# Performance work log

Measured on AMD Instinct MI355X. Metric: run time of the kernel, lower is better.

Reference implementation:

```python
import jax, jax.numpy as jnp
import numpy as np

N_NODES = 50000
N_EDGES = 800000
IN_DIM = 128
HIDDEN = 128
NUM_CLASSES = 64
NEG_SLOPE = 0.2


def setup_inputs() -> dict:
    key = jax.random.key(0)
    ks = jax.random.split(key, 12)
    x = jax.random.normal(ks[0], (N_NODES, IN_DIM), dtype=jnp.float32)
    src = jax.random.randint(ks[1], (N_EDGES,), 0, N_NODES, dtype=jnp.int64)
    dst = jax.random.randint(ks[2], (N_EDGES,), 0, N_NODES, dtype=jnp.int64)
    def glorot(k, shape):
        fan_in, fan_out = shape[0], shape[-1]
        s = jnp.sqrt(2.0 / (fan_in + fan_out)).astype(jnp.float32)
        return jax.random.normal(k, shape, dtype=jnp.float32) * s
    return {
        "x": x, "src": src, "dst": dst,
        # GATConv params (1 head, no bias, no residual)
        "W_gat": glorot(ks[3], (IN_DIM, HIDDEN)),
        "attn_l": glorot(ks[4], (HIDDEN,)),
        "attn_r": glorot(ks[5], (HIDDEN,)),
        # GraphConv params (norm='none', bias=True)
        "W1": glorot(ks[6], (HIDDEN, HIDDEN)),
        "b1": jnp.zeros((HIDDEN,), dtype=jnp.float32),
        "W2": glorot(ks[7], (HIDDEN, HIDDEN)),
        "b2": jnp.zeros((HIDDEN,), dtype=jnp.float32),
        "Wc": glorot(ks[8], (HIDDEN, NUM_CLASSES)),
        "bc": jnp.zeros((NUM_CLASSES,), dtype=jnp.float32),
    }


def reference(x, src, dst, W_gat, attn_l, attn_r, W1, b1, W2, b2, Wc, bc):
    N = x.shape[0]
    # --- GATConv, single head, eval mode (dropout=0) ---
    h = x @ W_gat                      # (N, H)
    el = h @ attn_l                    # (N,)
    er = h @ attn_r                    # (N,)
    e = jax.nn.leaky_relu(el[src] + er[dst], negative_slope=NEG_SLOPE)  # (E,)
    # edge softmax over incoming edges of each dst node
    emax = jax.ops.segment_max(e, dst, num_segments=N)
    ee = jnp.exp(e - emax[dst])
    esum = jax.ops.segment_sum(ee, dst, num_segments=N)
    alpha = ee / esum[dst]             # (E,) attention = reused edge weights
    h1 = jax.ops.segment_sum(h[src] * alpha[:, None], dst, num_segments=N)
    h1 = jax.nn.elu(h1)                # GATConv activation

    # --- GraphConv (norm='none') with edge_weight = alpha ---
    def gconv(hin, W, b):
        hp = hin @ W                                   # project (order is math-equivalent)
        agg = jax.ops.segment_sum(hp[src] * alpha[:, None], dst, num_segments=N)
        return agg + b

    h2 = gconv(h1, W1, b1)
    h3 = gconv(h2, W2, b2)
    logits = gconv(h3, Wc, bc)         # (N, num_classes)
    return logits
```

## Files before the change

### kernel.cpp

```cpp
#include <hip/hip_runtime.h>
#include <hip/hip_fp16.h>
#include <math.h>

#define N_NODES 50000
#define N_EDGES 800000
#define PAD_EDGES (N_EDGES + 8 * N_NODES)

typedef _Float16 half8 __attribute__((ext_vector_type(8)));
typedef float floatx16 __attribute__((ext_vector_type(16)));

__global__ __launch_bounds__(256) void prep_a_k(const float* __restrict__ Wg,
                                                const float* __restrict__ W1,
                                                const float* __restrict__ W2,
                                                const float* __restrict__ b1,
                                                __half* __restrict__ Wg_hl,
                                                float* __restrict__ W12,
                                                float* __restrict__ c12) {
  int e = blockIdx.x * 256 + threadIdx.x;
  if (e < 16384) {
    _Float16* o = (_Float16*)Wg_hl;
    int k = e >> 7, n = e & 127;
    float w = Wg[k * 128 + n];
    _Float16 hi = (_Float16)w;
    float lo = w - (float)hi;
    int oi = (((k >> 3) * 128 + n) << 3) | (k & 7);
    o[oi] = hi;
    o[16384 + oi] = (_Float16)lo;
  } else if (e < 32768) {
    int local = e - 16384;
    int k = local >> 7, n = local & 127;
    float acc = 0.f;
    for (int j = 0; j < 128; ++j) acc = fmaf(W1[k * 128 + j], W2[j * 128 + n], acc);
    W12[k * 128 + n] = acc;
  } else if (e < 32896) {
    int n = e - 32768;
    float acc = 0.f;
    for (int j = 0; j < 128; ++j) acc = fmaf(b1[j], W2[j * 128 + n], acc);
    c12[n] = acc;
  }
}

__global__ __launch_bounds__(256) void prepP_k(const float* __restrict__ W12,
                                               const float* __restrict__ c12,
                                               const float* __restrict__ Wc,
                                               const float* __restrict__ b2,
                                               __half* __restrict__ WPhl,
                                               float* __restrict__ c1,
                                               float* __restrict__ c2) {
  int e = blockIdx.x * 256 + threadIdx.x;
  _Float16* o = (_Float16*)WPhl;
  if (e < 8192) {
    int k = e >> 6, n = e & 63;
    float acc = 0.f;
    for (int j = 0; j < 128; ++j) acc = fmaf(W12[k * 128 + j], Wc[j * 64 + n], acc);
    _Float16 hi = (_Float16)acc;
    float lo = acc - (float)hi;
    int oi = (((k >> 3) * 64 + n) << 3) | (k & 7);
    o[oi] = hi;
    o[8192 + oi] = (_Float16)lo;
  } else if (e < 8256) {
    int n = e - 8192;
    float acc = 0.f;
    for (int j = 0; j < 128; ++j) acc = fmaf(c12[j], Wc[j * 64 + n], acc);
    c1[n] = acc;
  } else if (e < 8320) {
    int n = e - 8256;
    float acc = 0.f;
    for (int j = 0; j < 128; ++j) acc = fmaf(b2[j], Wc[j * 64 + n], acc);
    c2[n] = acc;
  }
}

template <int NCOL, bool A16, bool ELR>
__global__ __launch_bounds__(256) void mgemm_k(const void* __restrict__ Ap,
                                               const __half* __restrict__ Whl,
                                               __half* __restrict__ C16, int M,
                                               const float* __restrict__ al,
                                               const float* __restrict__ ar,
                                               float* __restrict__ el,
                                               float* __restrict__ er) {
  __shared__ __half Al[16][129][8];
  const int tid  = threadIdx.x;
  const int row0 = blockIdx.x * 128;
  const int lane = tid & 63;
  const int lane31 = lane & 31;
  const int q = lane >> 5;
  const int r = tid >> 6;

  if (A16) {
    const uint4* A8 = (const uint4*)Ap;
    #pragma unroll
    for (int i = 0; i < 8; ++i) {
      int idx = tid + i * 256;
      int row = idx >> 4, c = idx & 15;
      int grow = row0 + row;
      uint4 v = make_uint4(0u, 0u, 0u, 0u);
      if (grow < M) v = A8[grow * 16 + c];
      *reinterpret_cast<uint4*>(&Al[c][row][0]) = v;
    }
  } else {
    const float4* A4 = (const float4*)Ap;
    #pragma unroll
    for (int i = 0; i < 8; ++i) {
      int idx = tid + i * 256;
      int row = idx >> 4, c = idx & 15;
      int grow = row0 + row;
      half8 hv = {};
      if (grow < M) {
        float4 a0 = A4[grow * 32 + c * 2];
        float4 a1 = A4[grow * 32 + c * 2 + 1];
        hv[0] = (_Float16)a0.x; hv[1] = (_Float16)a0.y;
        hv[2] = (_Float16)a0.z; hv[3] = (_Float16)a0.w;
        hv[4] = (_Float16)a1.x; hv[5] = (_Float16)a1.y;
        hv[6] = (_Float16)a1.z; hv[7] = (_Float16)a1.w;
      }
      *reinterpret_cast<half8*>(&Al[c][row][0]) = hv;
    }
  }
  __syncthreads();

  half8 afr[8];
  #pragma unroll
  for (int s = 0; s < 8; ++s)
    afr[s] = *reinterpret_cast<const half8*>(&Al[2 * s + q][r * 32 + lane31][0]);

  const half8* B8 = reinterpret_cast<const half8*>(Whl);
  const int KN8 = 16 * NCOL;

  float elp[16], erp[16];
  if (ELR) {
    #pragma unroll
    for (int i = 0; i < 16; ++i) { elp[i] = 0.f; erp[i] = 0.f; }
  }

  #pragma unroll
  for (int tc = 0; tc < NCOL / 32; ++tc) {
    floatx16 acc = {};
    int nbase = tc * 32 + lane31;
    #pragma unroll
    for (int s = 0; s < 8; ++s) {
      int ci = (2 * s + q) * NCOL + nbase;
      half8 bl = B8[KN8 + ci];
      half8 bh = B8[ci];
      acc = __builtin_amdgcn_mfma_f32_32x32x16_f16(afr[s], bl, acc, 0, 0, 0);
      acc = __builtin_amdgcn_mfma_f32_32x32x16_f16(afr[s], bh, acc, 0, 0, 0);
    }
    if (ELR) {
      float alv = al[nbase], arv = ar[nbase];
      #pragma unroll
      for (int i = 0; i < 16; ++i) {
        elp[i] = fmaf(acc[i], alv, elp[i]);
        erp[i] = fmaf(acc[i], arv, erp[i]);
      }
    }
    #pragma unroll
    for (int i = 0; i < 16; ++i) {
      int rl = (i & 3) + 8 * (i >> 2) + 4 * q;
      int grow = row0 + r * 32 + rl;
      if (grow < M) C16[grow * NCOL + nbase] = __float2half(acc[i]);
    }
  }

  if (ELR) {
    #pragma unroll
    for (int off = 1; off <= 16; off <<= 1) {
      #pragma unroll
      for (int i = 0; i < 16; ++i) {
        elp[i] += __shfl_xor(elp[i], off);
        erp[i] += __shfl_xor(erp[i], off);
      }
    }
    if (lane31 == 0) {
      #pragma unroll
      for (int i = 0; i < 16; ++i) {
        int rl = (i & 3) + 8 * (i >> 2) + 4 * q;
        int grow = row0 + r * 32 + rl;
        if (grow < M) { el[grow] = elp[i]; er[grow] = erp[i]; }
      }
    }
  }
}

__global__ __launch_bounds__(256) void hist_k(const int* __restrict__ dst,
                                              int* __restrict__ deg,
                                              int* __restrict__ rank, int E) {
  int e = blockIdx.x * 256 + threadIdx.x;
  if (e < E) rank[e] = atomicAdd(&deg[dst[e]], 1);
}

__global__ __launch_bounds__(256) void scan1_k(const int* __restrict__ deg,
                                               int* __restrict__ offs,
                                               int* __restrict__ bsum, int N) {
  __shared__ int s[256];
  int t = threadIdx.x;
  int i = blockIdx.x * 256 + t;
  int v = 0;
  if (i < N) {
    int d = deg[i];
    v = (d + 7) & ~7;
    if (v < 8) v = 8;
  }
  s[t] = v;
  __syncthreads();
  for (int o = 1; o < 256; o <<= 1) {
    int add = (t >= o) ? s[t - o] : 0;
    __syncthreads();
    s[t] += add;
    __syncthreads();
  }
  if (i < N) offs[i] = s[t] - v;
  if (t == 255) bsum[blockIdx.x] = s[255];
}

__global__ __launch_bounds__(256) void scan2_k(int* __restrict__ bsum, int nb) {
  __shared__ int s[256];
  int t = threadIdx.x;
  int v = (t < nb) ? bsum[t] : 0;
  s[t] = v;
  __syncthreads();
  for (int o = 1; o < 256; o <<= 1) {
    int add = (t >= o) ? s[t - o] : 0;
    __syncthreads();
    s[t] += add;
    __syncthreads();
  }
  if (t < nb) bsum[t] = s[t] - v;
}

__global__ __launch_bounds__(256) void scan3_k(int* __restrict__ offs,
                                               const int* __restrict__ deg,
                                               const int* __restrict__ bsum,
                                               const float* __restrict__ el,
                                               float2* __restrict__ el2, int N) {
  int i = blockIdx.x * 256 + threadIdx.x;
  if (i < N) {
    int o = offs[i] + bsum[blockIdx.x];
    offs[i] = o;
    int d = deg[i];
    el2[i] = make_float2(el[i], (d > 0) ? 1.f : 0.f);
    if (i == N - 1) {
      int pd = (d + 7) & ~7;
      if (pd < 8) pd = 8;
      offs[N] = o + pd;
    }
  }
}

__global__ __launch_bounds__(256) void scatter_k(const int* __restrict__ src,
                                                 const int* __restrict__ dst,
                                                 const int* __restrict__ offs,
                                                 const int* __restrict__ rank,
                                                 int* __restrict__ csr_src, int E) {
  int e = blockIdx.x * 256 + threadIdx.x;
  if (e < E) {
    csr_src[offs[dst[e]] + rank[e]] = src[e];
  }
}

__device__ inline void fma8(float2 acc[4], uint4 u, float a) {
  __half2* h = reinterpret_cast<__half2*>(&u);
  #pragma unroll
  for (int j = 0; j < 4; ++j) {
    float2 f = __half22float2(h[j]);
    acc[j].x = fmaf(a, f.x, acc[j].x);
    acc[j].y = fmaf(a, f.y, acc[j].y);
  }
}

__global__ __launch_bounds__(256) void aggsm_k(const int* __restrict__ offs,
                                               const int* __restrict__ deg,
                                               const int* __restrict__ csr_src,
                                               const float2* __restrict__ el2,
                                               const float* __restrict__ er,
                                               int2* __restrict__ meta,
                                               float* __restrict__ t,
                                               const __half* __restrict__ hp,
                                               __half* __restrict__ out, int N) {
  __shared__ int2 lmeta[4][64];
  int wv   = threadIdx.x >> 6;
  int w    = (blockIdx.x * 256 + threadIdx.x) >> 6;
  int lane = threadIdx.x & 63;
  if (w >= N) return;
  int o0   = offs[w];
  int pcnt = offs[w + 1] - o0;
  int cnt  = deg[w];
  int q  = lane >> 4;
  int fl = lane & 15;
  const uint4* hpq = reinterpret_cast<const uint4*>(hp);

  if (cnt <= 64) {
    bool valid = lane < cnt;
    float erv = er[w];
    int s = 0;
    float ev = -3.4e38f, flag = 0.f;
    if (valid) {
      s = csr_src[o0 + lane];
      float2 e2 = el2[s];
      float e0 = e2.x + erv;
      ev = (e0 >= 0.f) ? e0 : 0.2f * e0;
      flag = e2.y;
    }
    float m = ev;
    #pragma unroll
    for (int off = 32; off; off >>= 1) m = fmaxf(m, __shfl_xor(m, off));
    float ee = valid ? __expf(ev - m) : 0.f;
    float sum = ee, tp = ee * flag;
    #pragma unroll
    for (int off = 32; off; off >>= 1) {
      sum += __shfl_xor(sum, off);
      tp  += __shfl_xor(tp, off);
    }
    float inv = (cnt > 0) ? 1.f / sum : 0.f;
    int2 mm = make_int2(0, 0);
    if (valid) mm = make_int2(s * 16, __float_as_int(ee * inv));
    if (lane < pcnt) meta[o0 + lane] = mm;
    lmeta[wv][lane] = mm;
    if (lane == 0) t[w] = tp * inv;
  } else {
    float erv = er[w];
    float m = -3.4e38f;
    for (int i = lane; i < cnt; i += 64) {
      int s = csr_src[o0 + i];
      float2 e2 = el2[s];
      float ev = e2.x + erv;
      ev = (ev >= 0.f) ? ev : 0.2f * ev;
      m = fmaxf(m, ev);
    }
    #pragma unroll
    for (int off = 32; off; off >>= 1) m = fmaxf(m, __shfl_xor(m, off));
    float sum = 0.f, tacc = 0.f;
    int myS = 0; float myE = 0.f;
    for (int i = lane; i < cnt; i += 64) {
      int s = csr_src[o0 + i];
      float2 e2 = el2[s];
      float ev = e2.x + erv;
      ev = (ev >= 0.f) ? ev : 0.2f * ev;
      float ee = __expf(ev - m);
      meta[o0 + i] = make_int2(s * 16, __float_as_int(ee));
      sum += ee;
      tacc += ee * e2.y;
      if (i == lane) { myS = s; myE = ee; }
    }
    #pragma unroll
    for (int off = 32; off; off >>= 1) {
      sum  += __shfl_xor(sum, off);
      tacc += __shfl_xor(tacc, off);
    }
    float inv = 1.f / sum;
    if (lane == 0) t[w] = tacc * inv;
    for (int i = lane; i < cnt; i += 64) {
      int2 mm = meta[o0 + i];
      meta[o0 + i] = make_int2(mm.x, __float_as_int(__int_as_float(mm.y) * inv));
    }
    for (int i = cnt + lane; i < pcnt; i += 64) meta[o0 + i] = make_int2(0, 0);
    lmeta[wv][lane] = make_int2(myS * 16, __float_as_int(myE * inv));
  }

  float2 acc0[4] = {}, acc1[4] = {};
  int pc = pcnt < 64 ? pcnt : 64;
  int2 mA = lmeta[wv][q], mB = lmeta[wv][4 + q];
  for (int base = 8; base < pc; base += 8) {
    int2 nA = lmeta[wv][base + q], nB = lmeta[wv][base + 4 + q];
    uint4 vA = hpq[mA.x + fl], vB = hpq[mB.x + fl];
    fma8(acc0, vA, __int_as_float(mA.y));
    fma8(acc1, vB, __int_as_float(mB.y));
    mA = nA; mB = nB;
  }
  {
    uint4 vA = hpq[mA.x + fl], vB = hpq[mB.x + fl];
    fma8(acc0, vA, __int_as_float(mA.y));
    fma8(acc1, vB, __int_as_float(mB.y));
  }
  for (int p = o0 + 64 + q; p < o0 + pcnt; p += 4) {
    int2 mm = meta[p];
    fma8(acc0, hpq[mm.x + fl], __int_as_float(mm.y));
  }
  #pragma unroll
  for (int j = 0; j < 4; ++j) { acc0[j].x += acc1[j].x; acc0[j].y += acc1[j].y; }
  #pragma unroll
  for (int off = 16; off <= 32; off <<= 1) {
    #pragma unroll
    for (int j = 0; j < 4; ++j) {
      acc0[j].x += __shfl_xor(acc0[j].x, off);
      acc0[j].y += __shfl_xor(acc0[j].y, off);
    }
  }
  if (q == 0) {
    float o8[8];
    #pragma unroll
    for (int j = 0; j < 4; ++j) { o8[2 * j] = acc0[j].x; o8[2 * j + 1] = acc0[j].y; }
    #pragma unroll
    for (int j = 0; j < 8; ++j) o8[j] = (o8[j] > 0.f) ? o8[j] : (__expf(o8[j]) - 1.f);
    __half2 p0 = __floats2half2_rn(o8[0], o8[1]);
    __half2 p1 = __floats2half2_rn(o8[2], o8[3]);
    __half2 p2 = __floats2half2_rn(o8[4], o8[5]);
    __half2 p3 = __floats2half2_rn(o8[6], o8[7]);
    uint4 pk;
    pk.x = *reinterpret_cast<unsigned*>(&p0);
    pk.y = *reinterpret_cast<unsigned*>(&p1);
    pk.z = *reinterpret_cast<unsigned*>(&p2);
    pk.w = *reinterpret_cast<unsigned*>(&p3);
    *reinterpret_cast<uint4*>(&out[w * 128 + fl * 8]) = pk;
  }
}

template <bool FINAL>
__global__ __launch_bounds__(256) void agg64v_k(const int* __restrict__ offs,
                                                const int2* __restrict__ meta,
                                                const __half* __restrict__ zp,
                                                const float* __restrict__ t,
                                                const int* __restrict__ deg,
                                                const float* __restrict__ c1,
                                                const float* __restrict__ c2,
                                                const float* __restrict__ bc,
                                                void* __restrict__ outp, int N) {
  int w    = (blockIdx.x * 256 + threadIdx.x) >> 6;
  int lane = threadIdx.x & 63;
  if (w >= N) return;
  int o0 = offs[w], o1 = offs[w + 1];
  int o   = lane >> 3;
  int fl  = lane & 7;
  const uint4* hpq = reinterpret_cast<const uint4*>(zp);

  float2 acc0[4] = {};
  int p = o0 + o;
  int2 mA = meta[p];
  for (; p + 8 < o1; p += 8) {
    int2 nA = meta[p + 8];
    uint4 vA = hpq[(mA.x >> 1) + fl];
    fma8(acc0, vA, __int_as_float(mA.y));
    mA = nA;
  }
  {
    uint4 vA = hpq[(mA.x >> 1) + fl];
    fma8(acc0, vA, __int_as_float(mA.y));
  }
  #pragma unroll
  for (int off = 8; off <= 32; off <<= 1) {
    #pragma unroll
    for (int j = 0; j < 4; ++j) {
      acc0[j].x += __shfl_xor(acc0[j].x, off);
      acc0[j].y += __shfl_xor(acc0[j].y, off);
    }
  }
  if (o == 0) {
    float o8[8];
    #pragma unroll
    for (int j = 0; j < 4; ++j) { o8[2 * j] = acc0[j].x; o8[2 * j + 1] = acc0[j].y; }
    if (FINAL) {
      float tw = t[w];
      float dw = (deg[w] > 0) ? 1.f : 0.f;
      float4 a0 = reinterpret_cast<const float4*>(c1)[fl * 2];
      float4 a1 = reinterpret_cast<const float4*>(c1)[fl * 2 + 1];
      float4 d0 = reinterpret_cast<const float4*>(c2)[fl * 2];
      float4 d1 = reinterpret_cast<const float4*>(c2)[fl * 2 + 1];
      float4 b0 = reinterpret_cast<const float4*>(bc)[fl * 2];
      float4 b1v = reinterpret_cast<const float4*>(bc)[fl * 2 + 1];
      o8[0] += tw * a0.x + dw * d0.x + b0.x;
      o8[1] += tw * a0.y + dw * d0.y + b0.y;
      o8[2] += tw * a0.z + dw * d0.z + b0.z;
      o8[3] += tw * a0.w + dw * d0.w + b0.w;
      o8[4] += tw * a1.x + dw * d1.x + b1v.x;
      o8[5] += tw * a1.y + dw * d1.y + b1v.y;
      o8[6] += tw * a1.z + dw * d1.z + b1v.z;
      o8[7] += tw * a1.w + dw * d1.w + b1v.w;
      float4* of = reinterpret_cast<float4*>(outp);
      of[w * 16 + fl * 2]     = make_float4(o8[0], o8[1], o8[2], o8[3]);
      of[w * 16 + fl * 2 + 1] = make_float4(o8[4], o8[5], o8[6], o8[7]);
    } else {
      __half2 p0 = __floats2half2_rn(o8[0], o8[1]);
      __half2 p1 = __floats2half2_rn(o8[2], o8[3]);
      __half2 p2 = __floats2half2_rn(o8[4], o8[5]);
      __half2 p3 = __floats2half2_rn(o8[6], o8[7]);
      uint4 pk;
      pk.x = *reinterpret_cast<unsigned*>(&p0);
      pk.y = *reinterpret_cast<unsigned*>(&p1);
      pk.z = *reinterpret_cast<unsigned*>(&p2);
      pk.w = *reinterpret_cast<unsigned*>(&p3);
      reinterpret_cast<uint4*>(outp)[w * 8 + fl] = pk;
    }
  }
}

extern "C" void kernel_launch(void* const* d_in, const int* in_sizes, int n_in,
                              void* d_out, int out_size, void* d_ws, size_t ws_size,
                              hipStream_t stream) {
  const float* x      = (const float*)d_in[0];
  const int*   src    = (const int*)d_in[1];
  const int*   dst    = (const int*)d_in[2];
  const float* W_gat  = (const float*)d_in[3];
  const float* attn_l = (const float*)d_in[4];
  const float* attn_r = (const float*)d_in[5];
  const float* W1     = (const float*)d_in[6];
  const float* b1     = (const float*)d_in[7];
  const float* W2     = (const float*)d_in[8];
  const float* b2     = (const float*)d_in[9];
  const float* Wc     = (const float*)d_in[10];
  const float* bc     = (const float*)d_in[11];
  float* out = (float*)d_out;

  char* ws = (char*)d_ws;
  size_t off = 0;
  auto walloc = [&](size_t bytes) -> void* {
    void* p = ws + off;
    off += (bytes + 255) & ~size_t(255);
    return p;
  };
  __half* P16     = (__half*)walloc((size_t)N_NODES * 128 * 2);
  __half* F16     = (__half*)walloc((size_t)N_NODES * 128 * 2);
  float*  el      = (float*)walloc((size_t)N_NODES * 4);
  float*  er      = (float*)walloc((size_t)N_NODES * 4);
  float2* el2     = (float2*)walloc((size_t)N_NODES * 8);
  float*  tbuf    = (float*)walloc((size_t)N_NODES * 4);
  int*    deg     = (int*)walloc((size_t)N_NODES * 4);
  int*    offs    = (int*)walloc((size_t)(N_NODES + 1) * 4);
  int*    rank    = (int*)walloc((size_t)N_EDGES * 4);
  int*    csr_src = (int*)walloc((size_t)PAD_EDGES * 4);
  int2*   meta    = (int2*)walloc((size_t)PAD_EDGES * 8);
  int*    bsum    = (int*)walloc(1024);
  __half* Wg_hl   = (__half*)walloc((size_t)32768 * 2);
  __half* WP_hl   = (__half*)walloc((size_t)16384 * 2);
  float*  W12     = (float*)walloc((size_t)16384 * 4);
  float*  c12     = (float*)walloc((size_t)128 * 4);
  float*  c1      = (float*)walloc((size_t)64 * 4);
  float*  c2      = (float*)walloc((size_t)64 * 4);

  hipMemsetAsync(deg, 0, (size_t)N_NODES * 4, stream);

  const dim3 blk(256);
  const int nwave_blocks = (N_NODES + 3) / 4;
  const int nedge_blocks = (N_EDGES + 255) / 256;
  const int nscan_blocks = (N_NODES + 255) / 256;
  const int ngemm_blocks = (N_NODES + 127) / 128;

  prep_a_k<<<dim3(129), blk, 0, stream>>>(W_gat, W1, W2, b1, Wg_hl, W12, c12);
  prepP_k<<<dim3(33), blk, 0, stream>>>(W12, c12, Wc, b2, WP_hl, c1, c2);

  mgemm_k<128, false, true><<<dim3(ngemm_blocks), blk, 0, stream>>>(
      x, Wg_hl, P16, N_NODES, attn_l, attn_r, el, er);

  hist_k<<<dim3(nedge_blocks), blk, 0, stream>>>(dst, deg, rank, N_EDGES);
  scan1_k<<<dim3(nscan_blocks), blk, 0, stream>>>(deg, offs, bsum, N_NODES);
  scan2_k<<<dim3(1), blk, 0, stream>>>(bsum, nscan_blocks);
  scan3_k<<<dim3(nscan_blocks), blk, 0, stream>>>(offs, deg, bsum, el, el2, N_NODES);
  scatter_k<<<dim3(nedge_blocks), blk, 0, stream>>>(src, dst, offs, rank, csr_src, N_EDGES);

  aggsm_k<<<dim3(nwave_blocks), blk, 0, stream>>>(offs, deg, csr_src, el2, er, meta, tbuf, P16, F16, N_NODES);
  mgemm_k<64, true, false><<<dim3(ngemm_blocks), blk, 0, stream>>>(
      F16, WP_hl, P16, N_NODES, nullptr, nullptr, nullptr, nullptr);
  agg64v_k<false><<<dim3(nwave_blocks), blk, 0, stream>>>(offs, meta, P16, nullptr, nullptr, nullptr, nullptr, nullptr, F16, N_NODES);
  agg64v_k<false><<<dim3(nwave_blocks), blk, 0, stream>>>(offs, meta, F16, nullptr, nullptr, nullptr, nullptr, nullptr, P16, N_NODES);
  agg64v_k<true><<<dim3(nwave_blocks), blk, 0, stream>>>(offs, meta, P16, tbuf, deg, c1, c2, bc, out, N_NODES);
}
```

Before: 284.0 us.

## Fuse scan passes, gather el into scatter, and dual-accumulate agg64v loop

Merges scan1 and scan2 into one kernel in which the last block to finish, found with an atomic counter, scans the block sums, saving one launch. The scatter kernel now gathers el2[src] and writes packed (src*16|flag, el) records straight into meta, so aggsm no longer does the dependent csr_src then el2 gather and the csr_src buffer is removed. The agg64v inner loop now processes two edges per iteration with separate accumulators instead of prefetching the next meta entry. The costs are a random el2 gather moved into scatter, a counter that must be zeroed through the enlarged memset, and a possible small register increase from the second accumulator.

After: 288.8 us. Within noise of the previous version (+1.7%).

```diff
diff --git a/kernel.cpp b/kernel.cpp
--- a/kernel.cpp
+++ b/kernel.cpp
@@ -188,10 +188,13 @@
   if (e < E) rank[e] = atomicAdd(&deg[dst[e]], 1);
 }
 
-__global__ __launch_bounds__(256) void scan1_k(const int* __restrict__ deg,
+__global__ __launch_bounds__(256) void scanA_k(const int* __restrict__ deg,
                                                int* __restrict__ offs,
-                                               int* __restrict__ bsum, int N) {
+                                               int* __restrict__ bsum,
+                                               int* __restrict__ counter,
+                                               int N, int nb) {
   __shared__ int s[256];
+  __shared__ int lastdone;
   int t = threadIdx.x;
   int i = blockIdx.x * 256 + t;
   int v = 0;
@@ -209,22 +212,26 @@
     __syncthreads();
   }
   if (i < N) offs[i] = s[t] - v;
-  if (t == 255) bsum[blockIdx.x] = s[255];
-}
-
-__global__ __launch_bounds__(256) void scan2_k(int* __restrict__ bsum, int nb) {
-  __shared__ int s[256];
-  int t = threadIdx.x;
-  int v = (t < nb) ? bsum[t] : 0;
-  s[t] = v;
+  if (t == 255) {
+    bsum[blockIdx.x] = s[255];
+    __threadfence();
+  }
   __syncthreads();
-  for (int o = 1; o < 256; o <<= 1) {
-    int add = (t >= o) ? s[t - o] : 0;
+  if (t == 0) lastdone = (atomicAdd(counter, 1) == nb - 1) ? 1 : 0;
+  __syncthreads();
+  if (lastdone) {
+    __threadfence();
+    int v2 = (t < nb) ? bsum[t] : 0;
+    s[t] = v2;
     __syncthreads();
-    s[t] += add;
-    __syncthreads();
-  }
-  if (t < nb) bsum[t] = s[t] - v;
+    for (int o = 1; o < 256; o <<= 1) {
+      int add = (t >= o) ? s[t - o] : 0;
+      __syncthreads();
+      s[t] += add;
+      __syncthreads();
+    }
+    if (t < nb) bsum[t] = s[t] - v2;
+  }
 }
 
 __global__ __launch_bounds__(256) void scan3_k(int* __restrict__ offs,
@@ -250,10 +257,15 @@
                                                  const int* __restrict__ dst,
                                                  const int* __restrict__ offs,
                                                  const int* __restrict__ rank,
-                                                 int* __restrict__ csr_src, int E) {
+                                                 const float2* __restrict__ el2,
+                                                 int2* __restrict__ meta, int E) {
   int e = blockIdx.x * 256 + threadIdx.x;
   if (e < E) {
-    csr_src[offs[dst[e]] + rank[e]] = src[e];
+    int v = dst[e], s = src[e];
+    float2 e2 = el2[s];
+    int pos = offs[v] + rank[e];
+    meta[pos] = make_int2((s * 16) | (e2.y != 0.f ? 1 : 0),
+                          __float_as_int(e2.x));
   }
 }
 
@@ -269,8 +281,6 @@
 
 __global__ __launch_bounds__(256) void aggsm_k(const int* __restrict__ offs,
                                                const int* __restrict__ deg,
-                                               const int* __restrict__ csr_src,
-                                               const float2* __restrict__ el2,
                                                const float* __restrict__ er,
                                                int2* __restrict__ meta,
                                                float* __restrict__ t,
@@ -291,14 +301,14 @@
   if (cnt <= 64) {
     bool valid = lane < cnt;
     float erv = er[w];
-    int s = 0;
+    int s16 = 0;
     float ev = -3.4e38f, flag = 0.f;
     if (valid) {
-      s = csr_src[o0 + lane];
-      float2 e2 = el2[s];
-      float e0 = e2.x + erv;
+      int2 mr = meta[o0 + lane];
+      s16 = mr.x & ~15;
+      flag = (float)(mr.x & 1);
+      float e0 = __int_as_float(mr.y) + erv;
       ev = (e0 >= 0.f) ? e0 : 0.2f * e0;
-      flag = e2.y;
     }
     float m = ev;
     #pragma unroll
@@ -312,7 +322,7 @@
     }
     float inv = (cnt > 0) ? 1.f / sum : 0.f;
     int2 mm = make_int2(0, 0);
-    if (valid) mm = make_int2(s * 16, __float_as_int(ee * inv));
+    if (valid) mm = make_int2(s16, __float_as_int(ee * inv));
     if (lane < pcnt) meta[o0 + lane] = mm;
     lmeta[wv][lane] = mm;
     if (lane == 0) t[w] = tp * inv;
@@ -320,26 +330,26 @@
     float erv = er[w];
     float m = -3.4e38f;
     for (int i = lane; i < cnt; i += 64) {
-      int s = csr_src[o0 + i];
-      float2 e2 = el2[s];
-      float ev = e2.x + erv;
+      int2 mr = meta[o0 + i];
+      float ev = __int_as_float(mr.y) + erv;
       ev = (ev >= 0.f) ? ev : 0.2f * ev;
       m = fmaxf(m, ev);
     }
     #pragma unroll
     for (int off = 32; off; off >>= 1) m = fmaxf(m, __shfl_xor(m, off));
     float sum = 0.f, tacc = 0.f;
-    int myS = 0; float myE = 0.f;
+    int myS16 = 0; float myE = 0.f;
     for (int i = lane; i < cnt; i += 64) {
-      int s = csr_src[o0 + i];
-      float2 e2 = el2[s];
-      float ev = e2.x + erv;
+      int2 mr = meta[o0 + i];
+      int s16 = mr.x & ~15;
+      float flag = (float)(mr.x & 1);
+      float ev = __int_as_float(mr.y) + erv;
       ev = (ev >= 0.f) ? ev : 0.2f * ev;
       float ee = __expf(ev - m);
-      meta[o0 + i] = make_int2(s * 16, __float_as_int(ee));
+      meta[o0 + i] = make_int2(s16, __float_as_int(ee));
       sum += ee;
-      tacc += ee * e2.y;
-      if (i == lane) { myS = s; myE = ee; }
+      tacc += ee * flag;
+      if (i == lane) { myS16 = s16; myE = ee; }
     }
     #pragma unroll
     for (int off = 32; off; off >>= 1) {
@@ -353,7 +363,7 @@
       meta[o0 + i] = make_int2(mm.x, __float_as_int(__int_as_float(mm.y) * inv));
     }
     for (int i = cnt + lane; i < pcnt; i += 64) meta[o0 + i] = make_int2(0, 0);
-    lmeta[wv][lane] = make_int2(myS * 16, __float_as_int(myE * inv));
+    lmeta[wv][lane] = make_int2(myS16, __float_as_int(myE * inv));
   }
 
   float2 acc0[4] = {}, acc1[4] = {};
@@ -422,19 +432,23 @@
   int fl  = lane & 7;
   const uint4* hpq = reinterpret_cast<const uint4*>(zp);
 
-  float2 acc0[4] = {};
+  float2 acc0[4] = {}, acc1[4] = {};
   int p = o0 + o;
-  int2 mA = meta[p];
-  for (; p + 8 < o1; p += 8) {
-    int2 nA = meta[p + 8];
+  for (; p + 8 < o1; p += 16) {
+    int2 mA = meta[p];
+    int2 mB = meta[p + 8];
+    uint4 vA = hpq[(mA.x >> 1) + fl];
+    uint4 vB = hpq[(mB.x >> 1) + fl];
+    fma8(acc0, vA, __int_as_float(mA.y));
+    fma8(acc1, vB, __int_as_float(mB.y));
+  }
+  if (p < o1) {
+    int2 mA = meta[p];
     uint4 vA = hpq[(mA.x >> 1) + fl];
     fma8(acc0, vA, __int_as_float(mA.y));
-    mA = nA;
-  }
-  {
-    uint4 vA = hpq[(mA.x >> 1) + fl];
-    fma8(acc0, vA, __int_as_float(mA.y));
-  }
+  }
+  #pragma unroll
+  for (int j = 0; j < 4; ++j) { acc0[j].x += acc1[j].x; acc0[j].y += acc1[j].y; }
   #pragma unroll
   for (int off = 8; off <= 32; off <<= 1) {
     #pragma unroll
@@ -512,10 +526,10 @@
   float*  er      = (float*)walloc((size_t)N_NODES * 4);
   float2* el2     = (float2*)walloc((size_t)N_NODES * 8);
   float*  tbuf    = (float*)walloc((size_t)N_NODES * 4);
-  int*    deg     = (int*)walloc((size_t)N_NODES * 4);
+  int*    deg     = (int*)walloc((size_t)(N_NODES + 64) * 4);
+  int*    counter = deg + N_NODES;
   int*    offs    = (int*)walloc((size_t)(N_NODES + 1) * 4);
   int*    rank    = (int*)walloc((size_t)N_EDGES * 4);
-  int*    csr_src = (int*)walloc((size_t)PAD_EDGES * 4);
   int2*   meta    = (int2*)walloc((size_t)PAD_EDGES * 8);
   int*    bsum    = (int*)walloc(1024);
   __half* Wg_hl   = (__half*)walloc((size_t)32768 * 2);
@@ -525,7 +539,7 @@
   float*  c1      = (float*)walloc((size_t)64 * 4);
   float*  c2      = (float*)walloc((size_t)64 * 4);
 
-  hipMemsetAsync(deg, 0, (size_t)N_NODES * 4, stream);
+  hipMemsetAsync(deg, 0, (size_t)(N_NODES + 64) * 4, stream);
 
   const dim3 blk(256);
   const int nwave_blocks = (N_NODES + 3) / 4;
@@ -540,12 +554,11 @@
       x, Wg_hl, P16, N_NODES, attn_l, attn_r, el, er);
 
   hist_k<<<dim3(nedge_blocks), blk, 0, stream>>>(dst, deg, rank, N_EDGES);
-  scan1_k<<<dim3(nscan_blocks), blk, 0, stream>>>(deg, offs, bsum, N_NODES);
-  scan2_k<<<dim3(1), blk, 0, stream>>>(bsum, nscan_blocks);
+  scanA_k<<<dim3(nscan_blocks), blk, 0, stream>>>(deg, offs, bsum, counter, N_NODES, nscan_blocks);
   scan3_k<<<dim3(nscan_blocks), blk, 0, stream>>>(offs, deg, bsum, el, el2, N_NODES);
-  scatter_k<<<dim3(nedge_blocks), blk, 0, stream>>>(src, dst, offs, rank, csr_src, N_EDGES);
-
-  aggsm_k<<<dim3(nwave_blocks), blk, 0, stream>>>(offs, deg, csr_src, el2, er, meta, tbuf, P16, F16, N_NODES);
+  scatter_k<<<dim3(nedge_blocks), blk, 0, stream>>>(src, dst, offs, rank, el2, meta, N_EDGES);
+
+  aggsm_k<<<dim3(nwave_blocks), blk, 0, stream>>>(offs, deg, er, meta, tbuf, P16, F16, N_NODES);
   mgemm_k<64, true, false><<<dim3(ngemm_blocks), blk, 0, stream>>>(
       F16, WP_hl, P16, N_NODES, nullptr, nullptr, nullptr, nullptr);
   agg64v_k<false><<<dim3(nwave_blocks), blk, 0, stream>>>(offs, meta, P16, nullptr, nullptr, nullptr, nullptr, nullptr, F16, N_NODES);
```
